# Optimization experiments

Hardware: AMD Instinct MI355X
Metric: run time of the kernel (lower is better)

The kernel has to match this reference:

```python
import jax, jax.numpy as jnp
import numpy as np
import math

B, T, C = 8, 1024, 512
H = 8
HD = C // H  # 64
MAX_REL = 64 + 4  # args.block_size + args.time_cond


def setup_inputs() -> dict:
    key = jax.random.key(0)
    ks = jax.random.split(key, 12)
    xavier = lambda k, shape: jax.random.uniform(
        k, shape, jnp.float32, -1.0, 1.0) * math.sqrt(6.0 / (shape[0] + shape[1]))
    return {
        "x": jax.random.normal(ks[0], (B, T, C), jnp.float32),
        "Wq": xavier(ks[1], (C, C)), "bq": jnp.zeros((C,), jnp.float32),
        "Wk": xavier(ks[2], (C, C)), "bk": jnp.zeros((C,), jnp.float32),
        "Wv": xavier(ks[3], (C, C)), "bv": jnp.zeros((C,), jnp.float32),
        "Wo": xavier(ks[4], (C, C)), "bo": jnp.zeros((C,), jnp.float32),
        "rel_k": xavier(ks[5], (2 * MAX_REL + 1, HD)),
        "rel_v": xavier(ks[6], (2 * MAX_REL + 1, HD)),
    }


def _rel_index(t):
    # clipped relative distance matrix, shifted to [0, 2*MAX_REL]
    r = jnp.arange(t)
    dist = jnp.clip(r[None, :] - r[:, None], -MAX_REL, MAX_REL)
    return dist + MAX_REL  # (T, T) int32


def reference(x, Wq, bq, Wk, bk, Wv, bv, Wo, bo, rel_k, rel_v):
    b, t, c = x.shape
    h, hd = H, HD
    q = x @ Wq + bq
    k = x @ Wk + bk
    v = x @ Wv + bv
    rq = q.reshape(b, t, h, hd).transpose(0, 2, 1, 3)  # (B,H,T,hd)
    rk = k.reshape(b, t, h, hd).transpose(0, 2, 1, 3)
    rv = v.reshape(b, t, h, hd).transpose(0, 2, 1, 3)

    idx = _rel_index(t)                 # (T,T)
    rk2 = rel_k[idx]                    # (T,T,hd)
    rv2 = rel_v[idx]                    # (T,T,hd)

    attn1 = jnp.einsum("bhqd,bhkd->bhqk", rq, rk)
    attn2 = jnp.einsum("bhqd,qkd->bhqk", rq, rk2)
    # NOTE: original scales by 1/sqrt(embed_dim) (k.size(-1) == C), not head_dim
    attn = jax.nn.softmax((attn1 + attn2) * (1.0 / math.sqrt(c)), axis=-1)

    w1 = jnp.einsum("bhqk,bhkd->bhqd", attn, rv)
    w2 = jnp.einsum("bhqk,qkd->bhqd", attn, rv2)
    out = (w1 + w2).transpose(0, 2, 1, 3).reshape(b, t, c)
    return out @ Wo + bo
```

## Files before the change

kernel.cpp:

```cpp
#include <hip/hip_runtime.h>
#include <stdint.h>

#define Bb 8
#define Tt 1024
#define Cc 512
#define Hh 8
#define HD 64
#define MREL 68
#define NR 137
#define NRP 160
#define A2S 168
#define SCALE 0.044194173824159216f
#define KSCL  0.063763016845703125f

typedef unsigned short u16;
typedef unsigned int u32;
using u16x4  = __attribute__((ext_vector_type(4))) u16;
using u16x8  = __attribute__((ext_vector_type(8))) u16;
using u32x2  = __attribute__((ext_vector_type(2))) u32;
using f32x4  = __attribute__((ext_vector_type(4))) float;
using bf16x8 = __attribute__((ext_vector_type(8))) __bf16;

__device__ __forceinline__ u16 f2bf(float f) {
  u32 u = __builtin_bit_cast(u32, f);
  u += 0x7FFF + ((u >> 16) & 1);
  return (u16)(u >> 16);
}
__device__ __forceinline__ float bf2f(u16 v) {
  return __builtin_bit_cast(float, (u32)v << 16);
}
__device__ __forceinline__ bf16x8 as_bf8(u16x8 v) { return __builtin_bit_cast(bf16x8, v); }
__device__ __forceinline__ float fexp2(float x) {
  float r; asm("v_exp_f32 %0, %1" : "=v"(r) : "v"(x)); return r;
}
__device__ __forceinline__ u32 cvtpk(float lo, float hi) {
  u32 r; asm("v_cvt_pk_bf16_f32 %0, %1, %2" : "=v"(r) : "v"(lo), "v"(hi)); return r;
}

#define MFMA16(a, b, c) __builtin_amdgcn_mfma_f32_16x16x32_bf16((a), (b), (c), 0, 0, 0)
#define PSWZ(row, col) ((col) ^ (((row) & 7) << 3))

__global__ __launch_bounds__(256) void relv_prep(
    const float* __restrict__ rel_v, u16* __restrict__ rvT)
{
  int i = blockIdx.x * 256 + threadIdx.x;
  if (i < HD * NRP) {
    int d = i / NRP, r = i - d * NRP;
    rvT[i] = (r < NR) ? f2bf(rel_v[r * HD + d]) : (u16)0;
  }
}

__global__ __launch_bounds__(256) void w_prep(
    const float* __restrict__ Wq, const float* __restrict__ Wk,
    const float* __restrict__ Wv, const float* __restrict__ Wo,
    u16* __restrict__ WqT, u16* __restrict__ WkT,
    u16* __restrict__ WvT, u16* __restrict__ WoT)
{
  const float* W = blockIdx.y == 0 ? Wq : blockIdx.y == 1 ? Wk
                  : blockIdx.y == 2 ? Wv : Wo;
  u16* WT = blockIdx.y == 0 ? WqT : blockIdx.y == 1 ? WkT
           : blockIdx.y == 2 ? WvT : WoT;
  int i = blockIdx.x * 256 + threadIdx.x;
  int n = i >> 7, k4 = (i & 127) * 4;
  u16x4 o;
  #pragma unroll
  for (int j = 0; j < 4; ++j) o[j] = f2bf(W[(size_t)(k4 + j) * Cc + n]);
  *(u16x4*)&WT[(size_t)n * Cc + k4] = o;
}

__global__ __launch_bounds__(256) void qkv_gemm(
    const float* __restrict__ x,
    const u16* __restrict__ WqT, const u16* __restrict__ WkT,
    const u16* __restrict__ WvT,
    const float* __restrict__ bq, const float* __restrict__ bk,
    const float* __restrict__ bv,
    u16* __restrict__ Qb, u16* __restrict__ Kb, u16* __restrict__ VTb)
{
  __shared__ u16 Xs[64][40];
  __shared__ u16 WTs[3][64][40];

  const u16* Wp[3] = {WqT, WkT, WvT};
  const float* bp[3] = {bq, bk, bv};

  const int tid = threadIdx.x;
  const int wv_ = tid >> 6;
  const int l   = tid & 63;
  const int lr  = l & 15, lg = l >> 4;
  const int m0  = blockIdx.x * 64;
  const int n0  = blockIdx.y * 64;
  const int srow = tid >> 2, scol = (tid & 3) * 8;

  f32x4 acc[3][4];
  #pragma unroll
  for (int a = 0; a < 3; ++a)
    #pragma unroll
    for (int b = 0; b < 4; ++b) acc[a][b] = (f32x4){0.f, 0.f, 0.f, 0.f};

  for (int k0 = 0; k0 < Cc; k0 += 32) {
    {
      const float* xp = x + (size_t)(m0 + srow) * Cc + k0 + scol;
      f32x4 v0 = *(const f32x4*)xp;
      f32x4 v1 = *(const f32x4*)(xp + 4);
      u16x8 o = {f2bf(v0[0]), f2bf(v0[1]), f2bf(v0[2]), f2bf(v0[3]),
                 f2bf(v1[0]), f2bf(v1[1]), f2bf(v1[2]), f2bf(v1[3])};
      *(u16x8*)&Xs[srow][scol] = o;
    }
    #pragma unroll
    for (int q3 = 0; q3 < 3; ++q3) {
      u16x8 w = *(const u16x8*)(Wp[q3] + (size_t)(n0 + srow) * Cc + k0 + scol);
      *(u16x8*)&WTs[q3][srow][scol] = w;
    }
    __syncthreads();

    bf16x8 a = as_bf8(*(const u16x8*)&Xs[wv_ * 16 + lr][lg * 8]);
    #pragma unroll
    for (int q3 = 0; q3 < 3; ++q3) {
      #pragma unroll
      for (int nt = 0; nt < 4; ++nt) {
        bf16x8 b = as_bf8(*(const u16x8*)&WTs[q3][nt * 16 + lr][lg * 8]);
        acc[q3][nt] = MFMA16(a, b, acc[q3][nt]);
      }
    }
    __syncthreads();
  }

  const int bidx = m0 >> 10;
  #pragma unroll
  for (int q3 = 0; q3 < 3; ++q3) {
    #pragma unroll
    for (int nt = 0; nt < 4; ++nt) {
      int n = n0 + nt * 16 + lr;
      int h = n >> 6, d = n & 63;
      float bias = bp[q3][n];
      #pragma unroll
      for (int i = 0; i < 4; ++i) {
        int m = m0 + wv_ * 16 + lg * 4 + i;
        int t = m & (Tt - 1);
        u16 o = f2bf(acc[q3][nt][i] + bias);
        size_t bh = (size_t)(bidx * Hh + h);
        if (q3 == 0)      Qb[(bh * Tt + t) * HD + d] = o;
        else if (q3 == 1) Kb[(bh * Tt + t) * HD + d] = o;
        else              VTb[(bh * HD + d) * Tt + t] = o;
      }
    }
  }
}

__global__ __launch_bounds__(256, 4) void attn_kernel(
    const u16* __restrict__ Qb, const u16* __restrict__ Kb,
    const u16* __restrict__ VTb, const u16* __restrict__ rvT,
    const float* __restrict__ rel_k,
    u16* __restrict__ AO)
{
  __shared__ u16 P[16][1024];
  __shared__ u16 S2a2[16][A2S];
  __shared__ float red[2][4][16];
  __shared__ float rowrcp[16];

  const int tid = threadIdx.x;
  const int wv_ = tid >> 6, l = tid & 63;
  const int lr = l & 15, lg = l >> 4;
  const int bh = blockIdx.x;
  const int q0 = blockIdx.y * 16;
  const int bidx = bh >> 3, h = bh & 7;

  const u16* Qh = Qb  + (size_t)bh * Tt * HD;
  const u16* Kh = Kb  + (size_t)bh * Tt * HD;
  const u16* Vh = VTb + (size_t)bh * HD * Tt;

  bf16x8 aQ0 = as_bf8(*(const u16x8*)(Qh + (size_t)(q0 + lr) * HD + lg * 8));
  bf16x8 aQ1 = as_bf8(*(const u16x8*)(Qh + (size_t)(q0 + lr) * HD + 32 + lg * 8));

  const u16* kbase = Kh + (size_t)(wv_ * 16 + lr) * HD + lg * 8;
  u16x8 c0 = *(const u16x8*)(kbase);
  u16x8 c1 = *(const u16x8*)(kbase + 32);

  for (int ct = wv_; ct < 9; ct += 4) {
    int r = ct * 16 + lr;
    f32x4 acc = {0.f, 0.f, 0.f, 0.f};
    #pragma unroll
    for (int d0 = 0; d0 < 64; d0 += 32) {
      u16x8 bbits = {0, 0, 0, 0, 0, 0, 0, 0};
      if (r < NR) {
        f32x4 v0 = *(const f32x4*)(rel_k + (size_t)r * HD + d0 + lg * 8);
        f32x4 v1 = *(const f32x4*)(rel_k + (size_t)r * HD + d0 + lg * 8 + 4);
        bbits = (u16x8){f2bf(v0[0]), f2bf(v0[1]), f2bf(v0[2]), f2bf(v0[3]),
                        f2bf(v1[0]), f2bf(v1[1]), f2bf(v1[2]), f2bf(v1[3])};
      }
      acc = MFMA16(d0 ? aQ1 : aQ0, as_bf8(bbits), acc);
    }
    #pragma unroll
    for (int i = 0; i < 4; ++i)
      S2a2[lg * 4 + i][ct * 16 + lr] = f2bf(acc[i] * KSCL);
  }
  __syncthreads();

  const int qme = q0 + lr;
  const float cN = bf2f(S2a2[lr][0]);
  const float cP = bf2f(S2a2[lr][NR - 1]);

  int lowEnd  = (q0 >= 131) ? (((q0 - 131) >> 6) + 1) : 0;
  int hiStart = (q0 + 146) >> 6; if (hiStart > 16) hiStart = 16;

  float ps = 0.f, ps0 = 0.f;
  const int kcb = wv_ * 16 + lg * 4;

  #pragma unroll
  for (int kt = 0; kt < 16; ++kt) {
    u16x8 n0{}, n1{};
    if (kt < 15) {
      n0 = *(const u16x8*)(kbase + (size_t)(kt + 1) * 64 * HD);
      n1 = *(const u16x8*)(kbase + (size_t)(kt + 1) * 64 * HD + 32);
    }
    f32x4 acc = {0.f, 0.f, 0.f, 0.f};
    acc = MFMA16(as_bf8(c0), aQ0, acc);
    acc = MFMA16(as_bf8(c1), aQ1, acc);
    int kc = kt * 64 + kcb;
    float p[4];
    if (kt >= lowEnd && kt < hiStart) {
      #pragma unroll
      for (int i = 0; i < 4; ++i) {
        int dr = kc + i - qme;
        dr = dr < -MREL ? -MREL : (dr > MREL ? MREL : dr);
        p[i] = fexp2(fmaf(acc[i], KSCL, bf2f(S2a2[lr][dr + MREL])));
        if (kc + i <= qme - MREL) ps0 += p[i];
      }
      ps += (p[0] + p[1]) + (p[2] + p[3]);
    } else {
      float c = (kt < lowEnd) ? cN : cP;
      #pragma unroll
      for (int i = 0; i < 4; ++i) p[i] = fexp2(fmaf(acc[i], KSCL, c));
      float s4 = (p[0] + p[1]) + (p[2] + p[3]);
      ps += s4;
      if (kt < lowEnd) ps0 += s4;
    }
    u32x2 pw = {cvtpk(p[0], p[1]), cvtpk(p[2], p[3])};
    *(u32x2*)&P[lr][PSWZ(lr, kc)] = pw;
    if (kt < 15) { c0 = n0; c1 = n1; }
  }

  ps  += __shfl_xor(ps, 16);  ps  += __shfl_xor(ps, 32);
  ps0 += __shfl_xor(ps0, 16); ps0 += __shfl_xor(ps0, 32);
  if (lg == 0) { red[0][wv_][lr] = ps; red[1][wv_][lr] = ps0; }

  const u16* vrow = Vh + (size_t)(wv_ * 16 + lr) * Tt + lg * 8;
  u16x8 vc0 = *(const u16x8*)(vrow);
  u16x8 vc1 = *(const u16x8*)(vrow + 32);

  __syncthreads();

  {
    int row = tid >> 4, c16 = tid & 15;
    int qg = q0 + row;
    float band = 0.f;
    for (int r = 1 + c16; r < NR - 1; r += 16) {
      int k = qg + r - MREL;
      u16 v = (k >= 0 && k < Tt) ? P[row][PSWZ(row, k)] : (u16)0;
      S2a2[row][r] = v;
      band += bf2f(v);
    }
    #pragma unroll
    for (int off = 1; off < 16; off <<= 1) band += __shfl_xor(band, off);
    for (int r = NR + c16; r < NRP; r += 16) S2a2[row][r] = 0;
    if (c16 == 0) {
      float t0 = red[0][0][row] + red[0][1][row] + red[0][2][row] + red[0][3][row];
      float t1 = red[1][0][row] + red[1][1][row] + red[1][2][row] + red[1][3][row];
      S2a2[row][0]      = f2bf(t1);
      S2a2[row][NR - 1] = f2bf(t0 - t1 - band);
      rowrcp[row] = 1.0f / t0;
    }
  }
  __syncthreads();

  f32x4 o0 = {0.f, 0.f, 0.f, 0.f}, o1 = {0.f, 0.f, 0.f, 0.f};
  #pragma unroll
  for (int kp = 0; kp < 15; ++kp) {
    u16x8 vn0 = *(const u16x8*)(vrow + kp * 64 + 64);
    u16x8 vn1 = *(const u16x8*)(vrow + kp * 64 + 96);
    bf16x8 a0 = as_bf8(*(const u16x8*)&P[lr][PSWZ(lr, kp * 64 + lg * 8)]);
    bf16x8 a1 = as_bf8(*(const u16x8*)&P[lr][PSWZ(lr, kp * 64 + 32 + lg * 8)]);
    o0 = MFMA16(a0, as_bf8(vc0), o0);
    o1 = MFMA16(a1, as_bf8(vc1), o1);
    vc0 = vn0; vc1 = vn1;
  }
  {
    bf16x8 a0 = as_bf8(*(const u16x8*)&P[lr][PSWZ(lr, 15 * 64 + lg * 8)]);
    bf16x8 a1 = as_bf8(*(const u16x8*)&P[lr][PSWZ(lr, 15 * 64 + 32 + lg * 8)]);
    o0 = MFMA16(a0, as_bf8(vc0), o0);
    o1 = MFMA16(a1, as_bf8(vc1), o1);
  }
  #pragma unroll
  for (int j = 0; j < 5; ++j) {
    u16x8 brv = *(const u16x8*)(rvT + (size_t)(wv_ * 16 + lr) * NRP + j * 32 + lg * 8);
    bf16x8 aa = as_bf8(*(const u16x8*)&S2a2[lr][j * 32 + lg * 8]);
    if (j & 1) o1 = MFMA16(aa, as_bf8(brv), o1);
    else       o0 = MFMA16(aa, as_bf8(brv), o0);
  }

  #pragma unroll
  for (int i = 0; i < 4; ++i) {
    int row = lg * 4 + i;
    float val = (o0[i] + o1[i]) * rowrcp[row];
    int t = q0 + row, cc = h * HD + wv_ * 16 + lr;
    AO[((size_t)(bidx * Tt + t)) * Cc + cc] = f2bf(val);
  }
}

__global__ __launch_bounds__(256) void out_gemm(
    const u16* __restrict__ AO, const u16* __restrict__ WoT,
    const float* __restrict__ bo, float* __restrict__ out)
{
  __shared__ u16 As[64][40];
  __shared__ u16 WTs[64][40];
  const int tid = threadIdx.x;
  const int wv_ = tid >> 6, l = tid & 63, lr = l & 15, lg = l >> 4;
  const int m0 = blockIdx.x * 64, n0 = blockIdx.y * 64;
  const int srow = tid >> 2, scol = (tid & 3) * 8;

  f32x4 acc[4];
  #pragma unroll
  for (int b = 0; b < 4; ++b) acc[b] = (f32x4){0.f, 0.f, 0.f, 0.f};

  for (int k0 = 0; k0 < Cc; k0 += 32) {
    u16x8 av = *(const u16x8*)(AO + (size_t)(m0 + srow) * Cc + k0 + scol);
    *(u16x8*)&As[srow][scol] = av;
    u16x8 wv2 = *(const u16x8*)(WoT + (size_t)(n0 + srow) * Cc + k0 + scol);
    *(u16x8*)&WTs[srow][scol] = wv2;
    __syncthreads();

    bf16x8 a = as_bf8(*(const u16x8*)&As[wv_ * 16 + lr][lg * 8]);
    #pragma unroll
    for (int nt = 0; nt < 4; ++nt) {
      bf16x8 b = as_bf8(*(const u16x8*)&WTs[nt * 16 + lr][lg * 8]);
      acc[nt] = MFMA16(a, b, acc[nt]);
    }
    __syncthreads();
  }

  #pragma unroll
  for (int nt = 0; nt < 4; ++nt) {
    int n = n0 + nt * 16 + lr;
    float bias = bo[n];
    #pragma unroll
    for (int i = 0; i < 4; ++i) {
      int m = m0 + wv_ * 16 + lg * 4 + i;
      out[(size_t)m * Cc + n] = acc[nt][i] + bias;
    }
  }
}

extern "C" void kernel_launch(void* const* d_in, const int* in_sizes, int n_in,
                              void* d_out, int out_size, void* d_ws, size_t ws_size,
                              hipStream_t stream) {
  const float* x  = (const float*)d_in[0];
  const float* Wq = (const float*)d_in[1];
  const float* bq = (const float*)d_in[2];
  const float* Wk = (const float*)d_in[3];
  const float* bk = (const float*)d_in[4];
  const float* Wv = (const float*)d_in[5];
  const float* bv = (const float*)d_in[6];
  const float* Wo = (const float*)d_in[7];
  const float* bo = (const float*)d_in[8];
  const float* rk = (const float*)d_in[9];
  const float* rv = (const float*)d_in[10];

  const size_t BHTD = (size_t)Bb * Hh * Tt * HD;
  const size_t WSZ  = (size_t)Cc * Cc;

  u16* Qb = (u16*)d_out;
  u16* Kb = Qb + BHTD;
  u16* VT  = (u16*)d_ws;
  u16* AO  = VT + BHTD;
  u16* rvT = AO + BHTD;
  u16* WqT = rvT + (size_t)HD * NRP;
  u16* WkT = WqT + WSZ;
  u16* WvT = WkT + WSZ;
  u16* WoT = WvT + WSZ;
  float* outf = (float*)d_out;

  relv_prep<<<dim3((HD * NRP + 255) / 256), 256, 0, stream>>>(rv, rvT);
  w_prep<<<dim3(256, 4), 256, 0, stream>>>(Wq, Wk, Wv, Wo, WqT, WkT, WvT, WoT);
  qkv_gemm<<<dim3(128, 8), 256, 0, stream>>>(x, WqT, WkT, WvT, bq, bk, bv, Qb, Kb, VT);
  attn_kernel<<<dim3(64, 64), 256, 0, stream>>>(Qb, Kb, VT, rvT, rk, AO);
  out_gemm<<<dim3(128, 8), 256, 0, stream>>>(AO, WoT, bo, outf);
}
```

Before: 209.1 us.

## Stream P through a small LDS buffer per key quarter and interleave PV MFMAs

The attention kernel no longer stores the full 16x1024 probability row block in LDS. It processes keys in four quarters, computing scores and exp, writing a 256-column P slice, then running the P·V MFMAs for that slice. Band probabilities for the rel_v term are scattered into a separate a2 buffer during the exp pass, and their sum is accumulated in registers, so the separate band-gather pass is removed. Less LDS use lets the launch bound rise to 6 blocks per CU for more occupancy. The cost is two extra block barriers per quarter, the loss of software prefetch of V rows, and dropping the P swizzle, which may cause LDS bank conflicts.

```diff
diff --git a/kernel.cpp b/kernel.cpp
--- a/kernel.cpp
+++ b/kernel.cpp
@@ -9,7 +9,6 @@
 #define MREL 68
 #define NR 137
 #define NRP 160
-#define A2S 168
 #define SCALE 0.044194173824159216f
 #define KSCL  0.063763016845703125f
 
@@ -38,7 +37,6 @@
 }
 
 #define MFMA16(a, b, c) __builtin_amdgcn_mfma_f32_16x16x32_bf16((a), (b), (c), 0, 0, 0)
-#define PSWZ(row, col) ((col) ^ (((row) & 7) << 3))
 
 __global__ __launch_bounds__(256) void relv_prep(
     const float* __restrict__ rel_v, u16* __restrict__ rvT)
@@ -146,15 +144,16 @@
   }
 }
 
-__global__ __launch_bounds__(256, 4) void attn_kernel(
+__global__ __launch_bounds__(256, 6) void attn_kernel(
     const u16* __restrict__ Qb, const u16* __restrict__ Kb,
     const u16* __restrict__ VTb, const u16* __restrict__ rvT,
     const float* __restrict__ rel_k,
     u16* __restrict__ AO)
 {
-  __shared__ u16 P[16][1024];
-  __shared__ u16 S2a2[16][A2S];
-  __shared__ float red[2][4][16];
+  __shared__ u16 P[16][264];
+  __shared__ u16 S2[16][144];
+  __shared__ u16 a2[16][168];
+  __shared__ float red[3][4][16];
   __shared__ float rowrcp[16];
 
   const int tid = threadIdx.x;
@@ -174,6 +173,8 @@
   const u16* kbase = Kh + (size_t)(wv_ * 16 + lr) * HD + lg * 8;
   u16x8 c0 = *(const u16x8*)(kbase);
   u16x8 c1 = *(const u16x8*)(kbase + 32);
+
+  for (int i = tid; i < 16 * 168 / 2; i += 256) ((u32*)a2)[i] = 0;
 
   for (int ct = wv_; ct < 9; ct += 4) {
     int r = ct * 16 + lr;
@@ -191,108 +192,95 @@
     }
     #pragma unroll
     for (int i = 0; i < 4; ++i)
-      S2a2[lg * 4 + i][ct * 16 + lr] = f2bf(acc[i] * KSCL);
+      S2[lg * 4 + i][ct * 16 + lr] = f2bf(acc[i] * KSCL);
   }
   __syncthreads();
 
   const int qme = q0 + lr;
-  const float cN = bf2f(S2a2[lr][0]);
-  const float cP = bf2f(S2a2[lr][NR - 1]);
+  const float cN = bf2f(S2[lr][0]);
+  const float cP = bf2f(S2[lr][NR - 1]);
 
   int lowEnd  = (q0 >= 131) ? (((q0 - 131) >> 6) + 1) : 0;
   int hiStart = (q0 + 146) >> 6; if (hiStart > 16) hiStart = 16;
 
-  float ps = 0.f, ps0 = 0.f;
+  float ps = 0.f, ps0 = 0.f, bnd = 0.f;
   const int kcb = wv_ * 16 + lg * 4;
-
-  #pragma unroll
-  for (int kt = 0; kt < 16; ++kt) {
-    u16x8 n0{}, n1{};
-    if (kt < 15) {
-      n0 = *(const u16x8*)(kbase + (size_t)(kt + 1) * 64 * HD);
-      n1 = *(const u16x8*)(kbase + (size_t)(kt + 1) * 64 * HD + 32);
-    }
-    f32x4 acc = {0.f, 0.f, 0.f, 0.f};
-    acc = MFMA16(as_bf8(c0), aQ0, acc);
-    acc = MFMA16(as_bf8(c1), aQ1, acc);
-    int kc = kt * 64 + kcb;
-    float p[4];
-    if (kt >= lowEnd && kt < hiStart) {
-      #pragma unroll
-      for (int i = 0; i < 4; ++i) {
-        int dr = kc + i - qme;
-        dr = dr < -MREL ? -MREL : (dr > MREL ? MREL : dr);
-        p[i] = fexp2(fmaf(acc[i], KSCL, bf2f(S2a2[lr][dr + MREL])));
-        if (kc + i <= qme - MREL) ps0 += p[i];
-      }
-      ps += (p[0] + p[1]) + (p[2] + p[3]);
-    } else {
-      float c = (kt < lowEnd) ? cN : cP;
-      #pragma unroll
-      for (int i = 0; i < 4; ++i) p[i] = fexp2(fmaf(acc[i], KSCL, c));
-      float s4 = (p[0] + p[1]) + (p[2] + p[3]);
-      ps += s4;
-      if (kt < lowEnd) ps0 += s4;
-    }
-    u32x2 pw = {cvtpk(p[0], p[1]), cvtpk(p[2], p[3])};
-    *(u32x2*)&P[lr][PSWZ(lr, kc)] = pw;
-    if (kt < 15) { c0 = n0; c1 = n1; }
+  const u16* vrow = Vh + (size_t)(wv_ * 16 + lr) * Tt + lg * 8;
+
+  f32x4 o0 = {0.f, 0.f, 0.f, 0.f}, o1 = {0.f, 0.f, 0.f, 0.f};
+
+  for (int qtr = 0; qtr < 4; ++qtr) {
+    #pragma unroll
+    for (int t = 0; t < 4; ++t) {
+      int kt = qtr * 4 + t;
+      u16x8 n0{}, n1{};
+      if (kt < 15) {
+        n0 = *(const u16x8*)(kbase + (size_t)(kt + 1) * 64 * HD);
+        n1 = *(const u16x8*)(kbase + (size_t)(kt + 1) * 64 * HD + 32);
+      }
+      f32x4 acc = {0.f, 0.f, 0.f, 0.f};
+      acc = MFMA16(as_bf8(c0), aQ0, acc);
+      acc = MFMA16(as_bf8(c1), aQ1, acc);
+      int kc = kt * 64 + kcb;
+      float p[4];
+      if (kt >= lowEnd && kt < hiStart) {
+        #pragma unroll
+        for (int i = 0; i < 4; ++i) {
+          int dr = kc + i - qme;
+          int drc = dr < -MREL ? -MREL : (dr > MREL ? MREL : dr);
+          float pe = fexp2(fmaf(acc[i], KSCL, bf2f(S2[lr][drc + MREL])));
+          p[i] = pe;
+          ps += pe;
+          if (dr <= -MREL) ps0 += pe;
+          if (dr >= -67 && dr <= 67) { a2[lr][dr + MREL] = f2bf(pe); bnd += pe; }
+        }
+      } else {
+        float c = (kt < lowEnd) ? cN : cP;
+        #pragma unroll
+        for (int i = 0; i < 4; ++i) p[i] = fexp2(fmaf(acc[i], KSCL, c));
+        float s4 = (p[0] + p[1]) + (p[2] + p[3]);
+        ps += s4;
+        if (kt < lowEnd) ps0 += s4;
+      }
+      u32x2 pw = {cvtpk(p[0], p[1]), cvtpk(p[2], p[3])};
+      *(u32x2*)&P[lr][t * 64 + kcb] = pw;
+      if (kt < 15) { c0 = n0; c1 = n1; }
+    }
+    __syncthreads();
+
+    #pragma unroll
+    for (int kp = 0; kp < 4; ++kp) {
+      int kpg = qtr * 4 + kp;
+      u16x8 vc0 = *(const u16x8*)(vrow + (size_t)kpg * 64);
+      u16x8 vc1 = *(const u16x8*)(vrow + (size_t)kpg * 64 + 32);
+      bf16x8 a0 = as_bf8(*(const u16x8*)&P[lr][kp * 64 + lg * 8]);
+      bf16x8 a1 = as_bf8(*(const u16x8*)&P[lr][kp * 64 + 32 + lg * 8]);
+      o0 = MFMA16(a0, as_bf8(vc0), o0);
+      o1 = MFMA16(a1, as_bf8(vc1), o1);
+    }
+    __syncthreads();
   }
 
   ps  += __shfl_xor(ps, 16);  ps  += __shfl_xor(ps, 32);
   ps0 += __shfl_xor(ps0, 16); ps0 += __shfl_xor(ps0, 32);
-  if (lg == 0) { red[0][wv_][lr] = ps; red[1][wv_][lr] = ps0; }
-
-  const u16* vrow = Vh + (size_t)(wv_ * 16 + lr) * Tt + lg * 8;
-  u16x8 vc0 = *(const u16x8*)(vrow);
-  u16x8 vc1 = *(const u16x8*)(vrow + 32);
-
+  bnd += __shfl_xor(bnd, 16); bnd += __shfl_xor(bnd, 32);
+  if (lg == 0) { red[0][wv_][lr] = ps; red[1][wv_][lr] = ps0; red[2][wv_][lr] = bnd; }
   __syncthreads();
 
-  {
-    int row = tid >> 4, c16 = tid & 15;
-    int qg = q0 + row;
-    float band = 0.f;
-    for (int r = 1 + c16; r < NR - 1; r += 16) {
-      int k = qg + r - MREL;
-      u16 v = (k >= 0 && k < Tt) ? P[row][PSWZ(row, k)] : (u16)0;
-      S2a2[row][r] = v;
-      band += bf2f(v);
-    }
-    #pragma unroll
-    for (int off = 1; off < 16; off <<= 1) band += __shfl_xor(band, off);
-    for (int r = NR + c16; r < NRP; r += 16) S2a2[row][r] = 0;
-    if (c16 == 0) {
-      float t0 = red[0][0][row] + red[0][1][row] + red[0][2][row] + red[0][3][row];
-      float t1 = red[1][0][row] + red[1][1][row] + red[1][2][row] + red[1][3][row];
-      S2a2[row][0]      = f2bf(t1);
-      S2a2[row][NR - 1] = f2bf(t0 - t1 - band);
-      rowrcp[row] = 1.0f / t0;
-    }
+  if (tid < 16) {
+    float t0 = red[0][0][tid] + red[0][1][tid] + red[0][2][tid] + red[0][3][tid];
+    float t1 = red[1][0][tid] + red[1][1][tid] + red[1][2][tid] + red[1][3][tid];
+    float tb = red[2][0][tid] + red[2][1][tid] + red[2][2][tid] + red[2][3][tid];
+    a2[tid][0]      = f2bf(t1);
+    a2[tid][NR - 1] = f2bf(t0 - t1 - tb);
+    rowrcp[tid] = 1.0f / t0;
   }
   __syncthreads();
 
-  f32x4 o0 = {0.f, 0.f, 0.f, 0.f}, o1 = {0.f, 0.f, 0.f, 0.f};
-  #pragma unroll
-  for (int kp = 0; kp < 15; ++kp) {
-    u16x8 vn0 = *(const u16x8*)(vrow + kp * 64 + 64);
-    u16x8 vn1 = *(const u16x8*)(vrow + kp * 64 + 96);
-    bf16x8 a0 = as_bf8(*(const u16x8*)&P[lr][PSWZ(lr, kp * 64 + lg * 8)]);
-    bf16x8 a1 = as_bf8(*(const u16x8*)&P[lr][PSWZ(lr, kp * 64 + 32 + lg * 8)]);
-    o0 = MFMA16(a0, as_bf8(vc0), o0);
-    o1 = MFMA16(a1, as_bf8(vc1), o1);
-    vc0 = vn0; vc1 = vn1;
-  }
-  {
-    bf16x8 a0 = as_bf8(*(const u16x8*)&P[lr][PSWZ(lr, 15 * 64 + lg * 8)]);
-    bf16x8 a1 = as_bf8(*(const u16x8*)&P[lr][PSWZ(lr, 15 * 64 + 32 + lg * 8)]);
-    o0 = MFMA16(a0, as_bf8(vc0), o0);
-    o1 = MFMA16(a1, as_bf8(vc1), o1);
-  }
   #pragma unroll
   for (int j = 0; j < 5; ++j) {
     u16x8 brv = *(const u16x8*)(rvT + (size_t)(wv_ * 16 + lr) * NRP + j * 32 + lg * 8);
-    bf16x8 aa = as_bf8(*(const u16x8*)&S2a2[lr][j * 32 + lg * 8]);
+    bf16x8 aa = as_bf8(*(const u16x8*)&a2[lr][j * 32 + lg * 8]);
     if (j & 1) o1 = MFMA16(aa, as_bf8(brv), o1);
     else       o0 = MFMA16(aa, as_bf8(brv), o0);
   }
```

After: 209.8 us, median of 4. Within noise of the previous version (+0.3%).
